# Optimization experiments

Measured on AMD Instinct MI355X. Metric: run time of the kernel, lower is better.

The kernel has to match this reference:

```python
import jax, jax.numpy as jnp
import numpy as np

B, T, H = 128, 2048, 512

def setup_inputs() -> dict:
    key = jax.random.key(0)
    k1, k2, k3, k4, k5 = jax.random.split(key, 5)
    scale = 1.0 / np.sqrt(H)
    return {
        "query": jax.random.normal(k1, (B, H), dtype=jnp.float32),
        "key": jax.random.normal(k2, (B, T, H), dtype=jnp.float32),
        "w1": jax.random.normal(k3, (H, H), dtype=jnp.float32) * scale,
        "w2": jax.random.normal(k4, (H, H), dtype=jnp.float32) * scale,
        "w_out": jax.random.normal(k5, (H,), dtype=jnp.float32) * scale,
    }

def reference(query, key, w1, w2, w_out):
    # attn_weight = w_out . tanh(relu(W1 q) + relu(W2 k)), softmax over T, weighted sum of key
    q_h = jax.nn.relu(jnp.einsum('bh,gh->bg', query, w1))            # (B, H)
    k_h = jax.nn.relu(jnp.einsum('bth,gh->btg', key, w2))            # (B, T, H)
    scores = jnp.einsum('btg,g->bt', jnp.tanh(q_h[:, None, :] + k_h), w_out)  # (B, T)
    attn = jax.nn.softmax(scores, axis=1)                            # (B, T)
    return jnp.einsum('bt,bth->bh', attn, key)                       # (B, H)
```

## Files before the change

kernel.cpp:

```cpp
#include <hip/hip_runtime.h>
#include <hip/hip_bf16.h>

#define B_N 128
#define T_N 2048
#define H_N 512

typedef __attribute__((ext_vector_type(8))) short bf16x8;
typedef __attribute__((ext_vector_type(4))) float f32x4;

union U4 { unsigned int i[4]; bf16x8 v; };

__device__ __forceinline__ unsigned int f2bf(float f) {
    unsigned int u = __float_as_uint(f);
    u += 0x7fffu + ((u >> 16) & 1u);
    return u >> 16;
}

__device__ __forceinline__ unsigned int cvtpk(float lo, float hi) {
    unsigned int r;
    asm("v_cvt_pk_bf16_f32 %0, %1, %2" : "=v"(r) : "v"(lo), "v"(hi));
    return r;
}

__device__ __forceinline__ float tanh_fast(float x) {
    float e = __expf(2.f * x);
    float r = __builtin_amdgcn_rcpf(e + 1.f);
    return 1.f - 2.f * r;
}

#define SCHED0 __builtin_amdgcn_sched_barrier(0)

__global__ void k_w2prep(const float* __restrict__ w2, unsigned short* __restrict__ w2sw) {
    int c = blockIdx.x * 256 + threadIdx.x;
    int g = c >> 6, kc = c & 63;
    const float4* s = reinterpret_cast<const float4*>(w2 + (size_t)g * H_N + kc * 8);
    float4 f0 = s[0], f1 = s[1];
    uint4 p;
    p.x = f2bf(f0.x) | (f2bf(f0.y) << 16);
    p.y = f2bf(f0.z) | (f2bf(f0.w) << 16);
    p.z = f2bf(f1.x) | (f2bf(f1.y) << 16);
    p.w = f2bf(f1.z) | (f2bf(f1.w) << 16);
    *reinterpret_cast<uint4*>(reinterpret_cast<char*>(w2sw) + (size_t)g * 1024 +
                              (((kc * 16) ^ ((g & 7) << 4)))) = p;
}

__global__ void k_qh(const float* __restrict__ query, const float* __restrict__ w1,
                     float* __restrict__ qh) {
    int b = blockIdx.x;
    int g = threadIdx.x;
    __shared__ float q[H_N];
    q[g] = query[(size_t)b * H_N + g];
    __syncthreads();
    const float4* w = reinterpret_cast<const float4*>(w1 + (size_t)g * H_N);
    float acc = 0.f;
#pragma unroll 4
    for (int i = 0; i < H_N / 4; ++i) {
        float4 wv = w[i];
        acc += q[4*i] * wv.x + q[4*i+1] * wv.y + q[4*i+2] * wv.z + q[4*i+3] * wv.w;
    }
    qh[(size_t)b * H_N + g] = fmaxf(acc, 0.f);
}

__global__ __launch_bounds__(512, 4) void k_scores(
    const float* __restrict__ key, const unsigned short* __restrict__ w2sw,
    const float* __restrict__ qh, const float* __restrict__ w_out,
    float* __restrict__ partial, float* __restrict__ psum)
{
    const int b    = blockIdx.y;
    const int chnk = blockIdx.x;
    const int t0   = chnk * 64;
    const int tid  = threadIdx.x;
    const int wid  = tid >> 6;
    const int lane = tid & 63;
    const int lrow = lane & 15;
    const int lq   = lane >> 4;
    const int wr   = wid >> 2;
    const int wc   = wid & 3;
    const int swz  = (lrow & 7) << 4;

    __shared__ __align__(16) char smem[81920];
    char* Bbuf  = smem;
    char* Abase = smem + 65536;
    float* sscore = reinterpret_cast<float*>(smem);
    float* wlds   = reinterpret_cast<float*>(smem + 2048);

    const char* keybB = reinterpret_cast<const char*>(key + ((size_t)b * T_N + t0) * H_N);
    const char* w2sb  = reinterpret_cast<const char*>(w2sw);

    const int arow = tid >> 3;
    const int acol = tid & 7;
    const char* asrc = keybB + (size_t)arow * 2048 + acol * 32;
    char* adst = Abase + arow * 128 + ((acol * 16) ^ ((arow & 7) << 4));

    float4 rA[2];

#define LOAD_A(u) do {                                           \
        const char* p_ = asrc + ((u) << 8);                      \
        rA[0] = *reinterpret_cast<const float4*>(p_);            \
        rA[1] = *reinterpret_cast<const float4*>(p_ + 16);       \
    } while (0)

#define WRITE_A(u) do {                                          \
        U4 u_;                                                   \
        u_.i[0] = cvtpk(rA[0].x, rA[0].y);                       \
        u_.i[1] = cvtpk(rA[0].z, rA[0].w);                       \
        u_.i[2] = cvtpk(rA[1].x, rA[1].y);                       \
        u_.i[3] = cvtpk(rA[1].z, rA[1].w);                       \
        *reinterpret_cast<bf16x8*>(adst + (((u) & 1) << 13)) = u_.v; \
    } while (0)

#define STAGE_B(u) do {                                          \
        _Pragma("unroll")                                        \
        for (int i_ = 0; i_ < 8; ++i_) {                         \
            int c0_ = i_ * 512 + wid * 64;                       \
            int c_  = c0_ + lane;                                \
            int row_ = c_ >> 3, slot_ = c_ & 7;                  \
            __builtin_amdgcn_global_load_lds(                    \
                (const __attribute__((address_space(1))) void*)(w2sb + (size_t)row_ * 1024 + ((u) << 7) + slot_ * 16), \
                (__attribute__((address_space(3))) void*)(Bbuf + c0_ * 16), 16, 0, 0); \
        }                                                        \
    } while (0)

    f32x4 acc[2][8];
#pragma unroll
    for (int m = 0; m < 2; ++m)
#pragma unroll
        for (int n = 0; n < 8; ++n) acc[m][n] = f32x4{0.f, 0.f, 0.f, 0.f};

    LOAD_A(0);
    asm volatile("s_waitcnt vmcnt(0)" ::: "memory");
    WRITE_A(0);
    STAGE_B(0);
    __syncthreads();

#pragma unroll 1
    for (int s = 0; s < 8; ++s) {
        if (s < 7) LOAD_A(s + 1);
        SCHED0;

        const char* Acur = Abase + ((s & 1) << 13);
#pragma unroll
        for (int ks = 0; ks < 2; ++ks) {
            bf16x8 av[2];
#pragma unroll
            for (int m = 0; m < 2; ++m) {
                int row = wr * 32 + m * 16 + lrow;
                av[m] = *reinterpret_cast<const bf16x8*>(
                    Acur + row * 128 + ((ks * 64 + lq * 16) ^ swz));
            }
#pragma unroll
            for (int nh = 0; nh < 2; ++nh) {
                bf16x8 bv[4];
#pragma unroll
                for (int j = 0; j < 4; ++j) {
                    int row = wc * 128 + (nh * 4 + j) * 16 + lrow;
                    bv[j] = *reinterpret_cast<const bf16x8*>(
                        Bbuf + row * 128 + ((ks * 64 + lq * 16) ^ swz));
                }
#pragma unroll
                for (int m = 0; m < 2; ++m)
#pragma unroll
                    for (int j = 0; j < 4; ++j)
                        acc[m][nh * 4 + j] = __builtin_amdgcn_mfma_f32_16x16x32_bf16(
                            av[m], bv[j], acc[m][nh * 4 + j], 0, 0, 0);
            }
        }
        __syncthreads();

        if (s < 7) {
            STAGE_B(s + 1);
            WRITE_A(s + 1);
        }
        __syncthreads();
    }

    float pscore[2][4] = {};
#pragma unroll
    for (int n = 0; n < 8; ++n) {
        int g = wc * 128 + n * 16 + lrow;
        float wo = w_out[g];
        float qv = qh[(size_t)b * H_N + g];
#pragma unroll
        for (int m = 0; m < 2; ++m)
#pragma unroll
            for (int r = 0; r < 4; ++r) {
                float x = qv + fmaxf(acc[m][n][r], 0.f);
                pscore[m][r] = fmaf(wo, tanh_fast(x), pscore[m][r]);
            }
    }

#pragma unroll
    for (int m = 0; m < 2; ++m)
#pragma unroll
        for (int r = 0; r < 4; ++r) {
            float v = pscore[m][r];
            v += __shfl_xor(v, 1);
            v += __shfl_xor(v, 2);
            v += __shfl_xor(v, 4);
            v += __shfl_xor(v, 8);
            if (lrow == 0)
                sscore[wc * 64 + wr * 32 + m * 16 + lq * 4 + r] = v;
        }
    __syncthreads();

    if (tid < 64)
        wlds[tid] = __expf(sscore[0 * 64 + tid] + sscore[1 * 64 + tid] +
                           sscore[2 * 64 + tid] + sscore[3 * 64 + tid]);
    __syncthreads();

    if (wid == 0) {
        float v = wlds[lane];
        v += __shfl_xor(v, 1);
        v += __shfl_xor(v, 2);
        v += __shfl_xor(v, 4);
        v += __shfl_xor(v, 8);
        v += __shfl_xor(v, 16);
        v += __shfl_xor(v, 32);
        if (lane == 0) psum[b * 32 + chnk] = v;
    }

    {
        const float* keyp = key + ((size_t)b * T_N + t0) * H_N + tid;
        float a0 = 0.f;
#pragma unroll 8
        for (int t = 0; t < 64; ++t)
            a0 = fmaf(wlds[t], keyp[(size_t)t * H_N], a0);
        partial[((size_t)(b * 32 + chnk)) * H_N + tid] = a0;
    }

#undef LOAD_A
#undef WRITE_A
#undef STAGE_B
}

__global__ void k_out(const float* __restrict__ partial, const float* __restrict__ psum,
                      float* __restrict__ out) {
    int idx = blockIdx.x * 256 + threadIdx.x;
    int b = idx >> 9, h = idx & 511;
    float s = 0.f, d = 0.f;
#pragma unroll
    for (int c = 0; c < 32; ++c) {
        s += partial[((size_t)(b * 32 + c)) * H_N + h];
        d += psum[b * 32 + c];
    }
    out[idx] = s / d;
}

extern "C" void kernel_launch(void* const* d_in, const int* in_sizes, int n_in,
                              void* d_out, int out_size, void* d_ws, size_t ws_size,
                              hipStream_t stream) {
    const float* query = (const float*)d_in[0];
    const float* key   = (const float*)d_in[1];
    const float* w1    = (const float*)d_in[2];
    const float* w2    = (const float*)d_in[3];
    const float* w_out = (const float*)d_in[4];
    float* out = (float*)d_out;

    char* ws = (char*)d_ws;
    unsigned short* w2sw = (unsigned short*)(ws);
    float* qh      = (float*)(ws + 524288);
    float* partial = (float*)(ws + 1048576);
    float* psum    = (float*)(ws + 9437184);

    hipLaunchKernelGGL(k_w2prep, dim3(128),     dim3(256), 0, stream, w2, w2sw);
    hipLaunchKernelGGL(k_qh,     dim3(128),     dim3(512), 0, stream, query, w1, qh);
    hipLaunchKernelGGL(k_scores, dim3(32, 128), dim3(512), 0, stream,
                       key, w2sw, qh, w_out, partial, psum);
    hipLaunchKernelGGL(k_out,    dim3(256),     dim3(256), 0, stream, partial, psum, out);
}
```

Measured before the change: 298.6 us.

## Double-buffer W2 tiles in LDS and fully unroll the K pipeline

Changes the W2 pre-swizzle layout so each 32-wide K slice is a contiguous 32KB block, then double-buffers B in LDS with two stages in flight. The main loop becomes 16 fully unrolled half-steps with explicit vmcnt/lgkmcnt waits and raw s_barriers in place of __syncthreads. The goal is to overlap the global-to-LDS weight loads and the key loads with MFMA work and to drop redundant waits. In exchange, correctness now depends on hand-counted vmcnt values, and the B fragment indexing was rewritten for the new layout.

```diff
diff --git a/kernel.cpp b/kernel.cpp
--- a/kernel.cpp
+++ b/kernel.cpp
@@ -28,20 +28,25 @@
     return 1.f - 2.f * r;
 }
 
-#define SCHED0 __builtin_amdgcn_sched_barrier(0)
+#define FENCE asm volatile("" ::: "memory")
+#define SBAR  do { FENCE; __builtin_amdgcn_s_barrier(); FENCE; } while (0)
+#define VMCNT(n) asm volatile("s_waitcnt vmcnt(" #n ")" ::: "memory")
+#define LGKM0    asm volatile("s_waitcnt lgkmcnt(0)" ::: "memory")
 
 __global__ void k_w2prep(const float* __restrict__ w2, unsigned short* __restrict__ w2sw) {
     int c = blockIdx.x * 256 + threadIdx.x;
-    int g = c >> 6, kc = c & 63;
-    const float4* s = reinterpret_cast<const float4*>(w2 + (size_t)g * H_N + kc * 8);
+    int g = c >> 6, sl8 = c & 63;
+    int kb = sl8 >> 2, lq = sl8 & 3;
+    const float4* s = reinterpret_cast<const float4*>(w2 + (size_t)g * H_N + kb * 32 + lq * 8);
     float4 f0 = s[0], f1 = s[1];
     uint4 p;
     p.x = f2bf(f0.x) | (f2bf(f0.y) << 16);
     p.y = f2bf(f0.z) | (f2bf(f0.w) << 16);
     p.z = f2bf(f1.x) | (f2bf(f1.y) << 16);
     p.w = f2bf(f1.z) | (f2bf(f1.w) << 16);
-    *reinterpret_cast<uint4*>(reinterpret_cast<char*>(w2sw) + (size_t)g * 1024 +
-                              (((kc * 16) ^ ((g & 7) << 4)))) = p;
+    int slot = (((g & 1) << 2) | lq) ^ ((g >> 1) & 7);
+    *reinterpret_cast<uint4*>(reinterpret_cast<char*>(w2sw) +
+                              kb * 32768 + (g >> 1) * 128 + (slot << 4)) = p;
 }
 
 __global__ void k_qh(const float* __restrict__ query, const float* __restrict__ w1,
@@ -76,10 +81,12 @@
     const int lq   = lane >> 4;
     const int wr   = wid >> 2;
     const int wc   = wid & 3;
-    const int swz  = (lrow & 7) << 4;
+    const int swzA = (lrow & 7) << 4;
+    const int rowB  = wc * 64 + (lrow >> 1);
+    const int slotB = ((((lrow & 1) << 2) | lq) ^ ((lrow >> 1) & 7)) << 4;
 
     __shared__ __align__(16) char smem[81920];
-    char* Bbuf  = smem;
+    char* Bbase = smem;
     char* Abase = smem + 65536;
     float* sscore = reinterpret_cast<float*>(smem);
     float* wlds   = reinterpret_cast<float*>(smem + 2048);
@@ -94,30 +101,31 @@
 
     float4 rA[2];
 
-#define LOAD_A(u) do {                                           \
-        const char* p_ = asrc + ((u) << 8);                      \
+#define LOAD_A(a) do {                                           \
+        const char* p_ = asrc + ((a) << 8);                      \
         rA[0] = *reinterpret_cast<const float4*>(p_);            \
         rA[1] = *reinterpret_cast<const float4*>(p_ + 16);       \
     } while (0)
 
-#define WRITE_A(u) do {                                          \
+#define WRITE_A(a) do {                                          \
         U4 u_;                                                   \
         u_.i[0] = cvtpk(rA[0].x, rA[0].y);                       \
         u_.i[1] = cvtpk(rA[0].z, rA[0].w);                       \
         u_.i[2] = cvtpk(rA[1].x, rA[1].y);                       \
         u_.i[3] = cvtpk(rA[1].z, rA[1].w);                       \
-        *reinterpret_cast<bf16x8*>(adst + (((u) & 1) << 13)) = u_.v; \
-    } while (0)
-
-#define STAGE_B(u) do {                                          \
+        *reinterpret_cast<bf16x8*>(adst + (((a) & 1) << 13)) = u_.v; \
+    } while (0)
+
+#define STAGE_B(kb) do {                                         \
+        char* dst_ = Bbase + (((kb) & 1) << 15);                 \
+        const char* src_ = w2sb + ((kb) << 15);                  \
         _Pragma("unroll")                                        \
-        for (int i_ = 0; i_ < 8; ++i_) {                         \
+        for (int i_ = 0; i_ < 4; ++i_) {                         \
             int c0_ = i_ * 512 + wid * 64;                       \
             int c_  = c0_ + lane;                                \
-            int row_ = c_ >> 3, slot_ = c_ & 7;                  \
             __builtin_amdgcn_global_load_lds(                    \
-                (const __attribute__((address_space(1))) void*)(w2sb + (size_t)row_ * 1024 + ((u) << 7) + slot_ * 16), \
-                (__attribute__((address_space(3))) void*)(Bbuf + c0_ * 16), 16, 0, 0); \
+                (const __attribute__((address_space(1))) void*)(src_ + c_ * 16), \
+                (__attribute__((address_space(3))) void*)(dst_ + c0_ * 16), 16, 0, 0); \
         }                                                        \
     } while (0)
 
@@ -127,52 +135,73 @@
 #pragma unroll
         for (int n = 0; n < 8; ++n) acc[m][n] = f32x4{0.f, 0.f, 0.f, 0.f};
 
+#define COMPUTE(s) do {                                                       \
+        const char* Acur_ = Abase + (((s >> 1) & 1) << 13);                   \
+        const char* Bcur_ = Bbase + (((s) & 1) << 15);                        \
+        const int kqa_ = ((s) & 1) * 64 + lq * 16;                            \
+        bf16x8 av_[2];                                                        \
+        _Pragma("unroll")                                                     \
+        for (int m_ = 0; m_ < 2; ++m_)                                        \
+            av_[m_] = *reinterpret_cast<const bf16x8*>(                       \
+                Acur_ + (wr * 32 + m_ * 16 + lrow) * 128 + (kqa_ ^ swzA));    \
+        _Pragma("unroll")                                                     \
+        for (int nh_ = 0; nh_ < 2; ++nh_) {                                   \
+            bf16x8 bv_[4];                                                    \
+            _Pragma("unroll")                                                 \
+            for (int j_ = 0; j_ < 4; ++j_)                                    \
+                bv_[j_] = *reinterpret_cast<const bf16x8*>(                   \
+                    Bcur_ + (rowB + (nh_ * 4 + j_) * 8) * 128 + slotB);       \
+            _Pragma("unroll")                                                 \
+            for (int m_ = 0; m_ < 2; ++m_)                                    \
+                _Pragma("unroll")                                             \
+                for (int j_ = 0; j_ < 4; ++j_)                                \
+                    acc[m_][nh_ * 4 + j_] = __builtin_amdgcn_mfma_f32_16x16x32_bf16( \
+                        av_[m_], bv_[j_], acc[m_][nh_ * 4 + j_], 0, 0, 0);    \
+        }                                                                     \
+    } while (0)
+
     LOAD_A(0);
-    asm volatile("s_waitcnt vmcnt(0)" ::: "memory");
+    STAGE_B(0);
+    STAGE_B(1);
+    VMCNT(8);
     WRITE_A(0);
-    STAGE_B(0);
-    __syncthreads();
-
-#pragma unroll 1
-    for (int s = 0; s < 8; ++s) {
-        if (s < 7) LOAD_A(s + 1);
-        SCHED0;
-
-        const char* Acur = Abase + ((s & 1) << 13);
-#pragma unroll
-        for (int ks = 0; ks < 2; ++ks) {
-            bf16x8 av[2];
-#pragma unroll
-            for (int m = 0; m < 2; ++m) {
-                int row = wr * 32 + m * 16 + lrow;
-                av[m] = *reinterpret_cast<const bf16x8*>(
-                    Acur + row * 128 + ((ks * 64 + lq * 16) ^ swz));
-            }
-#pragma unroll
-            for (int nh = 0; nh < 2; ++nh) {
-                bf16x8 bv[4];
-#pragma unroll
-                for (int j = 0; j < 4; ++j) {
-                    int row = wc * 128 + (nh * 4 + j) * 16 + lrow;
-                    bv[j] = *reinterpret_cast<const bf16x8*>(
-                        Bbuf + row * 128 + ((ks * 64 + lq * 16) ^ swz));
-                }
-#pragma unroll
-                for (int m = 0; m < 2; ++m)
-#pragma unroll
-                    for (int j = 0; j < 4; ++j)
-                        acc[m][nh * 4 + j] = __builtin_amdgcn_mfma_f32_16x16x32_bf16(
-                            av[m], bv[j], acc[m][nh * 4 + j], 0, 0, 0);
-            }
-        }
-        __syncthreads();
-
-        if (s < 7) {
-            STAGE_B(s + 1);
-            WRITE_A(s + 1);
-        }
-        __syncthreads();
-    }
+    VMCNT(4);
+    LGKM0;
+    SBAR;
+
+#define SLOT_EVEN(s) do {                                        \
+        COMPUTE(s);                                              \
+        SBAR;                                                    \
+        STAGE_B((s) + 2);                                        \
+        LOAD_A((s) / 2 + 1);                                     \
+        VMCNT(6);                             \
+        SBAR;                                                    \
+    } while (0)
+
+#define SLOT_ODD(s) do {                                         \
+        COMPUTE(s);                                              \
+        SBAR;                                                    \
+        STAGE_B((s) + 2);                                        \
+        VMCNT(4);               \
+        WRITE_A(((s) + 1) / 2);                                  \
+        LGKM0;                                                   \
+        SBAR;                                                    \
+    } while (0)
+
+    SLOT_EVEN(0);  SLOT_ODD(1);
+    SLOT_EVEN(2);  SLOT_ODD(3);
+    SLOT_EVEN(4);  SLOT_ODD(5);
+    SLOT_EVEN(6);  SLOT_ODD(7);
+    SLOT_EVEN(8);  SLOT_ODD(9);
+    SLOT_EVEN(10); SLOT_ODD(11);
+    SLOT_EVEN(12); SLOT_ODD(13);
+
+    COMPUTE(14);
+    SBAR;
+    VMCNT(0);
+    SBAR;
+    COMPUTE(15);
+    SBAR;
 
     float pscore[2][4] = {};
 #pragma unroll
@@ -231,6 +260,9 @@
 #undef LOAD_A
 #undef WRITE_A
 #undef STAGE_B
+#undef COMPUTE
+#undef SLOT_EVEN
+#undef SLOT_ODD
 }
 
 __global__ void k_out(const float* __restrict__ partial, const float* __restrict__ psum,
```

Measured after the change: 310.7 us. 1.04x slower.
